# Kernel tuning notes

Hardware: AMD Instinct MI355X
Metric: run time of the kernel (lower is better)

Reference implementation:

```python
import jax, jax.numpy as jnp
import numpy as np
import math

V, S, E, H, L, B = 50257, 1024, 768, 12, 12, 4
D = E // H
EPS = 1e-5


def setup_inputs() -> dict:
    key = jax.random.key(0)
    ks = jax.random.split(key, 20)
    sd = 0.02
    inp = {
        "idx": jax.random.randint(ks[0], (B, S), 0, V),
        "targets": jax.random.randint(ks[1], (B, S), 0, V),
        "wte": jax.random.normal(ks[2], (V, E), jnp.float32) * sd,  # tied with lm_head
        "wpe": jax.random.normal(ks[3], (S, E), jnp.float32) * sd,
        "ln1_g": jnp.ones((L, E), jnp.float32),
        "ln1_b": jnp.zeros((L, E), jnp.float32),
        "attn_w": jax.random.normal(ks[4], (L, E, 3 * E), jnp.float32) * sd,
        "attn_b": jnp.zeros((L, 3 * E), jnp.float32),
        "proj_w": jax.random.normal(ks[5], (L, E, E), jnp.float32) * (sd / math.sqrt(2 * L)),
        "proj_b": jnp.zeros((L, E), jnp.float32),
        "ln2_g": jnp.ones((L, E), jnp.float32),
        "ln2_b": jnp.zeros((L, E), jnp.float32),
        "fc_w": jax.random.normal(ks[6], (L, E, 4 * E), jnp.float32) * sd,
        "fc_b": jnp.zeros((L, 4 * E), jnp.float32),
        "fcp_w": jax.random.normal(ks[7], (L, 4 * E, E), jnp.float32) * (sd / math.sqrt(2 * L)),
        "fcp_b": jnp.zeros((L, E), jnp.float32),
        "lnf_g": jnp.ones((E,), jnp.float32),
        "lnf_b": jnp.zeros((E,), jnp.float32),
    }
    return inp


def layer_norm(x, g, b):
    mu = jnp.mean(x, axis=-1, keepdims=True)
    var = jnp.mean(jnp.square(x - mu), axis=-1, keepdims=True)
    return (x - mu) * jax.lax.rsqrt(var + EPS) * g + b


def reference(idx, targets, wte, wpe, ln1_g, ln1_b, attn_w, attn_b, proj_w, proj_b,
              ln2_g, ln2_b, fc_w, fc_b, fcp_w, fcp_b, lnf_g, lnf_b):
    seq = idx.shape[1]
    x = wte[idx] + wpe[:seq]  # [B,S,E]
    mask = jnp.tril(jnp.ones((seq, seq), bool))
    scale = 1.0 / math.sqrt(D)

    def block(x, p):
        l1g, l1b, aw, ab, pw, pb, l2g, l2b, fw, fb, fpw, fpb = p
        h = layer_norm(x, l1g, l1b)
        qkv = h @ aw + ab  # [B,S,3E]
        q, k, v = jnp.split(qkv, 3, axis=-1)
        q = q.reshape(-1, seq, H, D).transpose(0, 2, 1, 3)  # [B,H,S,D]
        k = k.reshape(-1, seq, H, D).transpose(0, 2, 1, 3)
        v = v.reshape(-1, seq, H, D).transpose(0, 2, 1, 3)
        scores = jnp.einsum('bhqd,bhkd->bhqk', q, k) * scale
        scores = jnp.where(mask, scores, -jnp.inf)
        attn = jax.nn.softmax(scores, axis=-1)
        y = jnp.einsum('bhqk,bhkd->bhqd', attn, v)
        y = y.transpose(0, 2, 1, 3).reshape(-1, seq, E)
        x = x + y @ pw + pb
        h2 = layer_norm(x, l2g, l2b)
        h2 = jax.nn.gelu(h2 @ fw + fb, approximate=False)
        x = x + h2 @ fpw + fpb
        return x, None

    x, _ = jax.lax.scan(block, x, (ln1_g, ln1_b, attn_w, attn_b, proj_w, proj_b,
                                   ln2_g, ln2_b, fc_w, fc_b, fcp_w, fcp_b))
    x = layer_norm(x, lnf_g, lnf_b)
    logits = x @ wte.T  # tied lm_head, [B,S,V]
    logp = jax.nn.log_softmax(logits, axis=-1)
    loss = -jnp.mean(jnp.take_along_axis(logp, targets[..., None], axis=-1))
    return logits, loss
```

## Files before the change

kernel.cpp:

```cpp
#include <hip/hip_runtime.h>
#include <hip/hip_bf16.h>
#include <math.h>

#define V 50257
#define SQ 1024
#define E 768
#define NH 12
#define NL 12
#define NB 4
#define MR (NB*SQ)

typedef __bf16 bf16x8 __attribute__((ext_vector_type(8)));
typedef float f32x4 __attribute__((ext_vector_type(4)));
typedef unsigned short us8 __attribute__((ext_vector_type(8)));

__device__ __forceinline__ float b2f(unsigned short u) {
    union { float f; unsigned int i; } x; x.i = ((unsigned int)u) << 16; return x.f;
}
__device__ __forceinline__ unsigned short f2b(float f) {
    unsigned int u = __float_as_uint(f);
    u = (u + 0x7fff + ((u >> 16) & 1)) >> 16;
    return (unsigned short)u;
}
__device__ __forceinline__ void gload16(const unsigned short* g, unsigned short* l) {
    __builtin_amdgcn_global_load_lds((const __attribute__((address_space(1))) void*)g,
                                     (__attribute__((address_space(3))) void*)l, 16, 0, 0);
}

__global__ __launch_bounds__(256)
void embed_k(const int* __restrict__ idx, const float* __restrict__ wte,
             const float* __restrict__ wpe, float* __restrict__ x)
{
    int r = blockIdx.x, t = threadIdx.x;
    int tok = idx[r];
    int s = r & (SQ - 1);
    const float* wt = wte + (size_t)tok * E;
    const float* wp = wpe + (size_t)s * E;
    float* xr = x + (size_t)r * E;
    for (int e = t; e < E; e += 256) xr[e] = wt[e] + wp[e];
}

__global__ __launch_bounds__(256)
void ln_k(const float* __restrict__ x, const float* __restrict__ g,
          const float* __restrict__ bb, unsigned short* __restrict__ out)
{
    int r = blockIdx.x, t = threadIdx.x;
    int lane = t & 63, wid = t >> 6;
    const float* xr = x + (size_t)r * E;
    float v0 = xr[t], v1 = xr[t + 256], v2 = xr[t + 512];
    float s = v0 + v1 + v2;
    #pragma unroll
    for (int o = 1; o < 64; o <<= 1) s += __shfl_xor(s, o);
    __shared__ float red[8];
    if (lane == 0) red[wid] = s;
    __syncthreads();
    float mu = (red[0] + red[1] + red[2] + red[3]) * (1.f / E);
    float d0 = v0 - mu, d1 = v1 - mu, d2 = v2 - mu;
    float s2 = d0 * d0 + d1 * d1 + d2 * d2;
    #pragma unroll
    for (int o = 1; o < 64; o <<= 1) s2 += __shfl_xor(s2, o);
    if (lane == 0) red[wid + 4] = s2;
    __syncthreads();
    float rs = rsqrtf((red[4] + red[5] + red[6] + red[7]) * (1.f / E) + 1e-5f);
    unsigned short* orow = out + (size_t)r * E;
    orow[t]       = f2b(d0 * rs * g[t] + bb[t]);
    orow[t + 256] = f2b(d1 * rs * g[t + 256] + bb[t + 256]);
    orow[t + 512] = f2b(d2 * rs * g[t + 512] + bb[t + 512]);
}

__global__ __launch_bounds__(256)
void conv_k(const float* __restrict__ in, unsigned short* __restrict__ out, int n4)
{
    int i = blockIdx.x * 256 + threadIdx.x;
    int stride = gridDim.x * 256;
    for (; i < n4; i += stride) {
        float4 v = ((const float4*)in)[i];
        ushort4 o;
        o.x = f2b(v.x); o.y = f2b(v.y); o.z = f2b(v.z); o.w = f2b(v.w);
        ((ushort4*)out)[i] = o;
    }
}

__global__ __launch_bounds__(256)
void tconv_k(const float* __restrict__ in, unsigned short* __restrict__ out, int Kd, int Nd)
{
    __shared__ float tile[32][33];
    size_t loff = (size_t)blockIdx.z * Kd * Nd;
    in  += loff;
    out += loff;
    int n0 = blockIdx.x * 32, k0 = blockIdx.y * 32;
    int tc = threadIdx.x & 31, tr = threadIdx.x >> 5;
    #pragma unroll
    for (int i = 0; i < 4; ++i)
        tile[tr + i * 8][tc] = in[(size_t)(k0 + tr + i * 8) * Nd + n0 + tc];
    __syncthreads();
    #pragma unroll
    for (int i = 0; i < 4; ++i)
        out[(size_t)(n0 + tr + i * 8) * Kd + k0 + tc] = f2b(tile[tc][tr + i * 8]);
}

template<int EPI, bool DB>
__global__ __launch_bounds__(256, 3)
void gemm_k(const unsigned short* __restrict__ A, const unsigned short* __restrict__ B,
            const float* __restrict__ bias, const float* __restrict__ resid,
            void* __restrict__ Cv, unsigned short* __restrict__ vt,
            float2* __restrict__ part, int M, int N, int K, int Nreal)
{
    constexpr int NBUF = DB ? 2 : 1;
    __shared__ __align__(16) unsigned short As[NBUF][128 * 64];
    __shared__ __align__(16) unsigned short Bs[NBUF][128 * 64];
    const int t = threadIdx.x;
    const int lane = t & 63, wv = t >> 6;
    const int wr = wv >> 1, wc = wv & 1;

    int m0, n0, ntile;
    if constexpr (EPI == 3) {
        int lin = blockIdx.y * gridDim.x + blockIdx.x;
        int cpx = (gridDim.x * gridDim.y) >> 3;
        int nl  = (lin & 7) * cpx + (lin >> 3);
        int mt  = nl & (gridDim.x - 1);
        ntile   = nl / gridDim.x;
        m0 = mt * 128; n0 = ntile * 128;
    } else {
        m0 = blockIdx.x * 128; n0 = blockIdx.y * 128; ntile = blockIdx.y;
    }
    const int lq = lane & 15, lg = lane >> 4;

    f32x4 acc[4][4];
    const f32x4 fz = {0.f, 0.f, 0.f, 0.f};
    #pragma unroll
    for (int i = 0; i < 4; ++i)
        #pragma unroll
        for (int j = 0; j < 4; ++j) acc[i][j] = fz;

    const int srow = t >> 3, sc = t & 7;

    auto stage = [&](int buf, int k0) {
        #pragma unroll
        for (int i = 0; i < 4; ++i) {
            int row = srow + i * 32;
            int gc = ((sc ^ (row & 7)) << 3);
            gload16(A + (size_t)(m0 + row) * K + k0 + gc, &As[buf][row * 64 + sc * 8]);
            int nrow = n0 + row;
            if (EPI == 3 && nrow >= Nreal) nrow = Nreal - 1;
            gload16(B + (size_t)nrow * K + k0 + gc, &Bs[buf][row * 64 + sc * 8]);
        }
    };
    auto compute = [&](int buf) {
        #pragma unroll
        for (int ks = 0; ks < 64; ks += 32) {
            bf16x8 af[4], bfr[4];
            #pragma unroll
            for (int mi = 0; mi < 4; ++mi) {
                int row = wr * 64 + mi * 16 + lq;
                int c = (ks >> 3) + lg;
                af[mi] = *(const bf16x8*)&As[buf][row * 64 + ((c ^ (row & 7)) << 3)];
            }
            #pragma unroll
            for (int ni = 0; ni < 4; ++ni) {
                int row = wc * 64 + ni * 16 + lq;
                int c = (ks >> 3) + lg;
                bfr[ni] = *(const bf16x8*)&Bs[buf][row * 64 + ((c ^ (row & 7)) << 3)];
            }
            #pragma unroll
            for (int mi = 0; mi < 4; ++mi)
                #pragma unroll
                for (int ni = 0; ni < 4; ++ni)
                    acc[mi][ni] = __builtin_amdgcn_mfma_f32_16x16x32_bf16(
                        af[mi], bfr[ni], acc[mi][ni], 0, 0, 0);
        }
    };

    const int KT = K >> 6;
    if constexpr (DB) {
        stage(0, 0);
        __syncthreads();
        int cur = 0;
        for (int kt = 0; kt < KT; ++kt) {
            if (kt + 1 < KT) stage(cur ^ 1, (kt + 1) << 6);
            compute(cur);
            __syncthreads();
            cur ^= 1;
        }
    } else {
        for (int kt = 0; kt < KT; ++kt) {
            stage(0, kt << 6);
            __syncthreads();
            compute(0);
            __syncthreads();
        }
    }

    const int colb = n0 + wc * 64 + lq;
    const int rowb = m0 + wr * 64 + lg * 4;

    if constexpr (EPI == 3) {
        __shared__ float2 Ls[2][64][2];
        float* C = (float*)Cv;
        #pragma unroll
        for (int mi = 0; mi < 4; ++mi) {
            #pragma unroll
            for (int j = 0; j < 4; ++j) {
                int row = rowb + mi * 16 + j;
                float v[4];
                #pragma unroll
                for (int ni = 0; ni < 4; ++ni) {
                    int col = colb + ni * 16;
                    float vv = acc[mi][ni][j];
                    if (col < Nreal) C[(size_t)row * Nreal + col] = vv;
                    else vv = -1e30f;
                    v[ni] = vv;
                }
                float lm = fmaxf(fmaxf(v[0], v[1]), fmaxf(v[2], v[3]));
                #pragma unroll
                for (int o = 1; o < 16; o <<= 1) lm = fmaxf(lm, __shfl_xor(lm, o));
                float ls = __expf(v[0] - lm) + __expf(v[1] - lm)
                         + __expf(v[2] - lm) + __expf(v[3] - lm);
                #pragma unroll
                for (int o = 1; o < 16; o <<= 1) ls += __shfl_xor(ls, o);
                if (lq == 0) Ls[wr][mi * 16 + lg * 4 + j][wc] = make_float2(lm, ls);
            }
        }
        __syncthreads();
        if (t < 128) {
            float2 a = Ls[t >> 6][t & 63][0];
            float2 b = Ls[t >> 6][t & 63][1];
            float mm = fmaxf(a.x, b.x);
            float ss = a.y * __expf(a.x - mm) + b.y * __expf(b.x - mm);
            part[(size_t)ntile * MR + m0 + t] = make_float2(mm, ss);
        }
    } else if constexpr (EPI == 0) {
        unsigned short* C = (unsigned short*)Cv;
        #pragma unroll
        for (int mi = 0; mi < 4; ++mi) {
            int r0 = rowb + mi * 16;
            #pragma unroll
            for (int ni = 0; ni < 4; ++ni) {
                int col = colb + ni * 16;
                float b4 = bias[col];
                float vals[4];
                #pragma unroll
                for (int j = 0; j < 4; ++j) vals[j] = acc[mi][ni][j] + b4;
                #pragma unroll
                for (int j = 0; j < 4; ++j)
                    C[(size_t)(r0 + j) * N + col] = f2b(vals[j]);
                if (col >= 2 * E) {
                    int d = col - 2 * E; int hh = d >> 6; d &= 63;
                    int bb2 = r0 >> 10, kv = r0 & (SQ - 1);
                    unsigned int lo = (unsigned int)f2b(vals[0]) | ((unsigned int)f2b(vals[1]) << 16);
                    unsigned int hi = (unsigned int)f2b(vals[2]) | ((unsigned int)f2b(vals[3]) << 16);
                    uint2 u; u.x = lo; u.y = hi;
                    *(uint2*)&vt[(((size_t)bb2 * NH + hh) * 64 + d) * SQ + kv] = u;
                }
            }
        }
    } else {
        #pragma unroll
        for (int mi = 0; mi < 4; ++mi) {
            #pragma unroll
            for (int ni = 0; ni < 4; ++ni) {
                int col = colb + ni * 16;
                #pragma unroll
                for (int j = 0; j < 4; ++j) {
                    int row = rowb + mi * 16 + j;
                    float v = acc[mi][ni][j] + bias[col];
                    if constexpr (EPI == 1) {
                        ((float*)Cv)[(size_t)row * N + col] =
                            v + resid[(size_t)row * N + col];
                    } else {
                        float u = v + 0.044715f * v * v * v;
                        float e = __expf(-1.5957691216f * u);
                        v = v / (1.f + e);
                        ((unsigned short*)Cv)[(size_t)row * N + col] = f2b(v);
                    }
                }
            }
        }
    }
}

__global__ __launch_bounds__(256)
void attn_k(const unsigned short* __restrict__ qkv, const unsigned short* __restrict__ vtg,
            unsigned short* __restrict__ y)
{
    const int bid = blockIdx.x;
    const int qb  = (SQ / 64 - 1) - (bid / 48);
    const int bh  = bid % 48;
    const int h = bh % NH, b = bh / NH;
    const int t = threadIdx.x, lane = t & 63, wid = t >> 6;
    const int q0 = qb * 64;
    const int lq = lane & 15, lg = lane >> 4;

    __shared__ __align__(16) unsigned short Ks[64 * 72];
    __shared__ __align__(16) unsigned short Vs[64 * 72];
    __shared__ __align__(16) unsigned short Ps[4][16 * 72];

    const unsigned short* base  = qkv + (size_t)b * SQ * 2304;
    const unsigned short* vbase = vtg + (size_t)bh * 64 * SQ;

    const int qrow = q0 + wid * 16 + lq;
    bf16x8 qf0 = *(const bf16x8*)(base + (size_t)qrow * 2304 + h * 64 + lg * 8);
    bf16x8 qf1 = *(const bf16x8*)(base + (size_t)qrow * 2304 + h * 64 + 32 + lg * 8);

    const int sr = t >> 3, sc = t & 7;
    us8 ka, kb, va, vb;
    {
        const unsigned short* kp = base + (size_t)sr * 2304 + 768 + h * 64 + sc * 8;
        ka = *(const us8*)kp;
        kb = *(const us8*)(kp + (size_t)32 * 2304);
        const unsigned short* vp = vbase + (size_t)sr * SQ + sc * 8;
        va = *(const us8*)vp;
        vb = *(const us8*)(vp + (size_t)32 * SQ);
    }

    f32x4 of[4];
    const f32x4 fz = {0.f, 0.f, 0.f, 0.f};
    #pragma unroll
    for (int i = 0; i < 4; ++i) of[i] = fz;
    float mreg = -1e30f, lreg = 0.f;

    for (int tt = 0; tt <= qb; ++tt) {
        __syncthreads();
        *(us8*)&Ks[sr * 72 + sc * 8] = ka;
        *(us8*)&Ks[(sr + 32) * 72 + sc * 8] = kb;
        *(us8*)&Vs[sr * 72 + sc * 8] = va;
        *(us8*)&Vs[(sr + 32) * 72 + sc * 8] = vb;
        __syncthreads();
        if (tt < qb) {
            int kv0n = (tt + 1) * 64;
            const unsigned short* kp = base + (size_t)(kv0n + sr) * 2304 + 768 + h * 64 + sc * 8;
            ka = *(const us8*)kp;
            kb = *(const us8*)(kp + (size_t)32 * 2304);
            const unsigned short* vp = vbase + (size_t)sr * SQ + kv0n + sc * 8;
            va = *(const us8*)vp;
            vb = *(const us8*)(vp + (size_t)32 * SQ);
        }

        f32x4 sf[4];
        #pragma unroll
        for (int mi = 0; mi < 4; ++mi) sf[mi] = fz;
        #pragma unroll
        for (int mi = 0; mi < 4; ++mi) {
            const unsigned short* kr = &Ks[(mi * 16 + lq) * 72 + lg * 8];
            bf16x8 k0 = *(const bf16x8*)kr;
            bf16x8 k1 = *(const bf16x8*)(kr + 32);
            sf[mi] = __builtin_amdgcn_mfma_f32_16x16x32_bf16(k0, qf0, sf[mi], 0, 0, 0);
            sf[mi] = __builtin_amdgcn_mfma_f32_16x16x32_bf16(k1, qf1, sf[mi], 0, 0, 0);
        }

        float pv[16];
        const int kvb = tt * 64 + lg * 4;
        #pragma unroll
        for (int mi = 0; mi < 4; ++mi)
            #pragma unroll
            for (int j = 0; j < 4; ++j) {
                float s = sf[mi][j] * 0.125f;
                if (tt == qb && (kvb + mi * 16 + j) > qrow) s = -1e30f;
                pv[mi * 4 + j] = s;
            }
        float tm = pv[0];
        #pragma unroll
        for (int i = 1; i < 16; ++i) tm = fmaxf(tm, pv[i]);
        tm = fmaxf(tm, __shfl_xor(tm, 16));
        tm = fmaxf(tm, __shfl_xor(tm, 32));
        float mn  = fmaxf(mreg, tm);
        float fac = __expf(mreg - mn);
        float ts = 0.f;
        #pragma unroll
        for (int i = 0; i < 16; ++i) { float p = __expf(pv[i] - mn); pv[i] = p; ts += p; }
        ts += __shfl_xor(ts, 16);
        ts += __shfl_xor(ts, 32);
        lreg = lreg * fac + ts;
        mreg = mn;
        #pragma unroll
        for (int j = 0; j < 4; ++j) {
            float fj = __shfl(fac, 20 * lg + j);
            of[0][j] *= fj; of[1][j] *= fj; of[2][j] *= fj; of[3][j] *= fj;
        }
        unsigned short* pw = &Ps[wid][lq * 72];
        #pragma unroll
        for (int mi = 0; mi < 4; ++mi) {
            unsigned int lo = (unsigned int)f2b(pv[mi * 4 + 0]) | ((unsigned int)f2b(pv[mi * 4 + 1]) << 16);
            unsigned int hi = (unsigned int)f2b(pv[mi * 4 + 2]) | ((unsigned int)f2b(pv[mi * 4 + 3]) << 16);
            uint2 u; u.x = lo; u.y = hi;
            *(uint2*)&pw[mi * 16 + lg * 4] = u;
        }
        #pragma unroll
        for (int ks = 0; ks < 2; ++ks) {
            bf16x8 pf = *(const bf16x8*)&Ps[wid][lq * 72 + ks * 32 + lg * 8];
            #pragma unroll
            for (int ni = 0; ni < 4; ++ni) {
                bf16x8 vf = *(const bf16x8*)&Vs[(ni * 16 + lq) * 72 + ks * 32 + lg * 8];
                of[ni] = __builtin_amdgcn_mfma_f32_16x16x32_bf16(pf, vf, of[ni], 0, 0, 0);
            }
        }
    }

    float inv = 1.f / lreg;
    #pragma unroll
    for (int j = 0; j < 4; ++j) {
        float fj = __shfl(inv, 20 * lg + j);
        int row = q0 + wid * 16 + lg * 4 + j;
        unsigned short* yr = y + ((size_t)b * SQ + row) * E + h * 64 + lq;
        #pragma unroll
        for (int ni = 0; ni < 4; ++ni)
            yr[ni * 16] = f2b(of[ni][j] * fj);
    }
}

__global__ __launch_bounds__(256)
void lossred_k(const float2* __restrict__ part, const float* __restrict__ logits,
               const int* __restrict__ tgt, float* __restrict__ rl, int NT)
{
    int t = threadIdx.x, lane = t & 63, wid = t >> 6;
    int r = blockIdx.x * 4 + wid;
    float m = -1e30f, s = 0.f;
    for (int nt = lane; nt < NT; nt += 64) {
        float2 p = part[(size_t)nt * MR + r];
        float mm = fmaxf(m, p.x);
        s = s * __expf(m - mm) + p.y * __expf(p.x - mm);
        m = mm;
    }
    #pragma unroll
    for (int o = 1; o < 64; o <<= 1) {
        float m2 = __shfl_xor(m, o), s2 = __shfl_xor(s, o);
        float mm = fmaxf(m, m2);
        s = s * __expf(m - mm) + s2 * __expf(m2 - mm);
        m = mm;
    }
    if (lane == 0)
        rl[r] = __logf(s) + m - logits[(size_t)r * V + tgt[r]];
}

__global__ __launch_bounds__(256)
void finloss_k(const float* __restrict__ rl, float* __restrict__ out)
{
    __shared__ float red[256];
    int t = threadIdx.x;
    float s = 0.f;
    for (int i = t; i < MR; i += 256) s += rl[i];
    red[t] = s; __syncthreads();
    for (int o = 128; o > 0; o >>= 1) { if (t < o) red[t] += red[t + o]; __syncthreads(); }
    if (t == 0) out[0] = red[0] * (1.f / MR);
}

extern "C" void kernel_launch(void* const* d_in, const int* in_sizes, int n_in,
                              void* d_out, int out_size, void* d_ws, size_t ws_size,
                              hipStream_t stream)
{
    const int*   idx    = (const int*)  d_in[0];
    const int*   tgt    = (const int*)  d_in[1];
    const float* wte    = (const float*)d_in[2];
    const float* wpe    = (const float*)d_in[3];
    const float* ln1_g  = (const float*)d_in[4];
    const float* ln1_b  = (const float*)d_in[5];
    const float* attn_w = (const float*)d_in[6];
    const float* attn_b = (const float*)d_in[7];
    const float* proj_w = (const float*)d_in[8];
    const float* proj_b = (const float*)d_in[9];
    const float* ln2_g  = (const float*)d_in[10];
    const float* ln2_b  = (const float*)d_in[11];
    const float* fc_w   = (const float*)d_in[12];
    const float* fc_b   = (const float*)d_in[13];
    const float* fcp_w  = (const float*)d_in[14];
    const float* fcp_b  = (const float*)d_in[15];
    const float* lnf_g  = (const float*)d_in[16];
    const float* lnf_b  = (const float*)d_in[17];

    unsigned char* p = (unsigned char*)d_ws;
    auto alloc = [&](size_t bytes) {
        unsigned char* r = p; p += (bytes + 255) & ~(size_t)255; return r;
    };
    float*          x    = (float*)         alloc((size_t)MR * E * 4);
    unsigned short* h    = (unsigned short*)alloc((size_t)MR * E * 2);
    unsigned short* qkv  = (unsigned short*)alloc((size_t)MR * 3 * E * 2);
    unsigned short* yb   = (unsigned short*)alloc((size_t)MR * E * 2);
    unsigned short* act  = (unsigned short*)alloc((size_t)MR * 4 * E * 2);
    unsigned short* wteb = (unsigned short*)alloc((size_t)V * E * 2);
    unsigned short* vtg  = (unsigned short*)alloc((size_t)NB * NH * 64 * SQ * 2);
    float2*         part = (float2*)        alloc((size_t)393 * MR * 8);
    float*          rl   = (float*)         alloc((size_t)MR * 4);

    size_t used = (size_t)(p - (unsigned char*)d_ws);
    size_t perL = (size_t)12 * E * E * 2 + 4 * 256;
    int NLW = (ws_size >= used + (size_t)NL * perL) ? NL : 1;
    unsigned short* wqA  = (unsigned short*)alloc((size_t)NLW * 3 * E * E * 2);
    unsigned short* wpA  = (unsigned short*)alloc((size_t)NLW * E * E * 2);
    unsigned short* wfA  = (unsigned short*)alloc((size_t)NLW * 4 * E * E * 2);
    unsigned short* wfpA = (unsigned short*)alloc((size_t)NLW * 4 * E * E * 2);

    float* logits = (float*)d_out;
    float* lossp  = logits + (size_t)MR * V;

    embed_k<<<MR, 256, 0, stream>>>(idx, wte, wpe, x);
    conv_k<<<2048, 256, 0, stream>>>(wte, wteb, (int)((size_t)V * E / 4));

    if (NLW == NL) {
        tconv_k<<<dim3(3 * E / 32, E / 32, NL), 256, 0, stream>>>(attn_w, wqA, E, 3 * E);
        tconv_k<<<dim3(E / 32, E / 32, NL), 256, 0, stream>>>(proj_w, wpA, E, E);
        tconv_k<<<dim3(4 * E / 32, E / 32, NL), 256, 0, stream>>>(fc_w, wfA, E, 4 * E);
        tconv_k<<<dim3(E / 32, 4 * E / 32, NL), 256, 0, stream>>>(fcp_w, wfpA, 4 * E, E);
    }

    for (int l = 0; l < NL; ++l) {
        int lw = (NLW == NL) ? l : 0;
        unsigned short* wq  = wqA  + (size_t)lw * 3 * E * E;
        unsigned short* wp  = wpA  + (size_t)lw * E * E;
        unsigned short* wf  = wfA  + (size_t)lw * 4 * E * E;
        unsigned short* wfp = wfpA + (size_t)lw * 4 * E * E;
        if (NLW != NL) {
            tconv_k<<<dim3(3 * E / 32, E / 32), 256, 0, stream>>>(
                attn_w + (size_t)l * E * 3 * E, wq, E, 3 * E);
            tconv_k<<<dim3(E / 32, E / 32), 256, 0, stream>>>(
                proj_w + (size_t)l * E * E, wp, E, E);
            tconv_k<<<dim3(4 * E / 32, E / 32), 256, 0, stream>>>(
                fc_w + (size_t)l * E * 4 * E, wf, E, 4 * E);
            tconv_k<<<dim3(E / 32, 4 * E / 32), 256, 0, stream>>>(
                fcp_w + (size_t)l * 4 * E * E, wfp, 4 * E, E);
        }

        ln_k<<<MR, 256, 0, stream>>>(x, ln1_g + l * E, ln1_b + l * E, h);
        gemm_k<0, false><<<dim3(32, 18), 256, 0, stream>>>(
            h, wq, attn_b + (size_t)l * 3 * E, nullptr, qkv, vtg, nullptr,
            MR, 3 * E, E, 3 * E);
        attn_k<<<768, 256, 0, stream>>>(qkv, vtg, yb);
        gemm_k<1, false><<<dim3(32, 6), 256, 0, stream>>>(
            yb, wp, proj_b + (size_t)l * E, x, x, nullptr, nullptr, MR, E, E, E);
        ln_k<<<MR, 256, 0, stream>>>(x, ln2_g + l * E, ln2_b + l * E, h);
        gemm_k<2, false><<<dim3(32, 24), 256, 0, stream>>>(
            h, wf, fc_b + (size_t)l * 4 * E, nullptr, act, nullptr, nullptr,
            MR, 4 * E, E, 4 * E);
        gemm_k<1, false><<<dim3(32, 6), 256, 0, stream>>>(
            act, wfp, fcp_b + (size_t)l * E, x, x, nullptr, nullptr, MR, E, 4 * E, E);
    }

    ln_k<<<MR, 256, 0, stream>>>(x, lnf_g, lnf_b, h);
    gemm_k<3, true><<<dim3(32, 393), 256, 0, stream>>>(
        h, wteb, nullptr, nullptr, logits, nullptr, part, MR, 50304, E, V);

    lossred_k<<<MR / 4, 256, 0, stream>>>(part, logits, tgt, rl, 393);
    finloss_k<<<1, 256, 0, stream>>>(rl, lossp);
}
```

Measured before the change: 3.066 ms.

## Parameterize GEMM tile shape; use smaller tiles for projections and wider LM-head tiles

Templates the GEMM on per-wave MI/NI fragment counts and a min-waves launch bound, so each call site can pick its tile shape. The two N=768 projection GEMMs move to 64x128 tiles, doubling their block count to fill more CUs. The LM-head GEMM moves to 128x256 tiles without double buffering or the grouped tile swizzle, which halves the number of partial softmax entries and the A re-reads. The trade-off is higher register pressure (launch bound of 2) and the loss of L2-friendly tile ordering and load/compute overlap in the largest GEMM.

```diff
diff --git a/kernel.cpp b/kernel.cpp
--- a/kernel.cpp
+++ b/kernel.cpp
@@ -99,48 +99,44 @@
         out[(size_t)(n0 + tr + i * 8) * Kd + k0 + tc] = f2b(tile[tc][tr + i * 8]);
 }
 
-template<int EPI, bool DB>
-__global__ __launch_bounds__(256, 3)
+template<int EPI, bool DB, int MI, int NI, int MINW>
+__global__ __launch_bounds__(256, MINW)
 void gemm_k(const unsigned short* __restrict__ A, const unsigned short* __restrict__ B,
             const float* __restrict__ bias, const float* __restrict__ resid,
             void* __restrict__ Cv, unsigned short* __restrict__ vt,
             float2* __restrict__ part, int M, int N, int K, int Nreal)
 {
     constexpr int NBUF = DB ? 2 : 1;
-    __shared__ __align__(16) unsigned short As[NBUF][128 * 64];
-    __shared__ __align__(16) unsigned short Bs[NBUF][128 * 64];
+    constexpr int BM = 32 * MI, BN = 32 * NI;
+    __shared__ __align__(16) unsigned short As[NBUF][BM * 64];
+    __shared__ __align__(16) unsigned short Bs[NBUF][BN * 64];
     const int t = threadIdx.x;
     const int lane = t & 63, wv = t >> 6;
     const int wr = wv >> 1, wc = wv & 1;
-
-    int m0, n0, ntile;
-    if constexpr (EPI == 3) {
-        int lin = blockIdx.y * gridDim.x + blockIdx.x;
-        int cpx = (gridDim.x * gridDim.y) >> 3;
-        int nl  = (lin & 7) * cpx + (lin >> 3);
-        int mt  = nl & (gridDim.x - 1);
-        ntile   = nl / gridDim.x;
-        m0 = mt * 128; n0 = ntile * 128;
-    } else {
-        m0 = blockIdx.x * 128; n0 = blockIdx.y * 128; ntile = blockIdx.y;
-    }
+    const int m0 = blockIdx.x * BM, n0 = blockIdx.y * BN;
+    const int ntile = blockIdx.y;
     const int lq = lane & 15, lg = lane >> 4;
 
-    f32x4 acc[4][4];
+    f32x4 acc[MI][NI];
     const f32x4 fz = {0.f, 0.f, 0.f, 0.f};
     #pragma unroll
-    for (int i = 0; i < 4; ++i)
-        #pragma unroll
-        for (int j = 0; j < 4; ++j) acc[i][j] = fz;
+    for (int i = 0; i < MI; ++i)
+        #pragma unroll
+        for (int j = 0; j < NI; ++j) acc[i][j] = fz;
 
     const int srow = t >> 3, sc = t & 7;
 
     auto stage = [&](int buf, int k0) {
         #pragma unroll
-        for (int i = 0; i < 4; ++i) {
+        for (int i = 0; i < MI; ++i) {
             int row = srow + i * 32;
             int gc = ((sc ^ (row & 7)) << 3);
             gload16(A + (size_t)(m0 + row) * K + k0 + gc, &As[buf][row * 64 + sc * 8]);
+        }
+        #pragma unroll
+        for (int i = 0; i < NI; ++i) {
+            int row = srow + i * 32;
+            int gc = ((sc ^ (row & 7)) << 3);
             int nrow = n0 + row;
             if (EPI == 3 && nrow >= Nreal) nrow = Nreal - 1;
             gload16(B + (size_t)nrow * K + k0 + gc, &Bs[buf][row * 64 + sc * 8]);
@@ -149,23 +145,23 @@
     auto compute = [&](int buf) {
         #pragma unroll
         for (int ks = 0; ks < 64; ks += 32) {
-            bf16x8 af[4], bfr[4];
-            #pragma unroll
-            for (int mi = 0; mi < 4; ++mi) {
-                int row = wr * 64 + mi * 16 + lq;
+            bf16x8 af[MI], bfr[NI];
+            #pragma unroll
+            for (int mi = 0; mi < MI; ++mi) {
+                int row = wr * (16 * MI) + mi * 16 + lq;
                 int c = (ks >> 3) + lg;
                 af[mi] = *(const bf16x8*)&As[buf][row * 64 + ((c ^ (row & 7)) << 3)];
             }
             #pragma unroll
-            for (int ni = 0; ni < 4; ++ni) {
-                int row = wc * 64 + ni * 16 + lq;
+            for (int ni = 0; ni < NI; ++ni) {
+                int row = wc * (16 * NI) + ni * 16 + lq;
                 int c = (ks >> 3) + lg;
                 bfr[ni] = *(const bf16x8*)&Bs[buf][row * 64 + ((c ^ (row & 7)) << 3)];
             }
             #pragma unroll
-            for (int mi = 0; mi < 4; ++mi)
-                #pragma unroll
-                for (int ni = 0; ni < 4; ++ni)
+            for (int mi = 0; mi < MI; ++mi)
+                #pragma unroll
+                for (int ni = 0; ni < NI; ++ni)
                     acc[mi][ni] = __builtin_amdgcn_mfma_f32_16x16x32_bf16(
                         af[mi], bfr[ni], acc[mi][ni], 0, 0, 0);
         }
@@ -191,40 +187,43 @@
         }
     }
 
-    const int colb = n0 + wc * 64 + lq;
-    const int rowb = m0 + wr * 64 + lg * 4;
+    const int colb = n0 + wc * (16 * NI) + lq;
+    const int rowb = m0 + wr * (16 * MI) + lg * 4;
 
     if constexpr (EPI == 3) {
-        __shared__ float2 Ls[2][64][2];
+        __shared__ float2 Ls[2][BM / 2][2];
         float* C = (float*)Cv;
         #pragma unroll
-        for (int mi = 0; mi < 4; ++mi) {
+        for (int mi = 0; mi < MI; ++mi) {
             #pragma unroll
             for (int j = 0; j < 4; ++j) {
                 int row = rowb + mi * 16 + j;
-                float v[4];
-                #pragma unroll
-                for (int ni = 0; ni < 4; ++ni) {
+                float v[NI];
+                #pragma unroll
+                for (int ni = 0; ni < NI; ++ni) {
                     int col = colb + ni * 16;
                     float vv = acc[mi][ni][j];
                     if (col < Nreal) C[(size_t)row * Nreal + col] = vv;
                     else vv = -1e30f;
                     v[ni] = vv;
                 }
-                float lm = fmaxf(fmaxf(v[0], v[1]), fmaxf(v[2], v[3]));
+                float lm = v[0];
+                #pragma unroll
+                for (int ni = 1; ni < NI; ++ni) lm = fmaxf(lm, v[ni]);
                 #pragma unroll
                 for (int o = 1; o < 16; o <<= 1) lm = fmaxf(lm, __shfl_xor(lm, o));
-                float ls = __expf(v[0] - lm) + __expf(v[1] - lm)
-                         + __expf(v[2] - lm) + __expf(v[3] - lm);
+                float ls = 0.f;
+                #pragma unroll
+                for (int ni = 0; ni < NI; ++ni) ls += __expf(v[ni] - lm);
                 #pragma unroll
                 for (int o = 1; o < 16; o <<= 1) ls += __shfl_xor(ls, o);
                 if (lq == 0) Ls[wr][mi * 16 + lg * 4 + j][wc] = make_float2(lm, ls);
             }
         }
         __syncthreads();
-        if (t < 128) {
-            float2 a = Ls[t >> 6][t & 63][0];
-            float2 b = Ls[t >> 6][t & 63][1];
+        if (t < BM) {
+            float2 a = Ls[t / (BM / 2)][t % (BM / 2)][0];
+            float2 b = Ls[t / (BM / 2)][t % (BM / 2)][1];
             float mm = fmaxf(a.x, b.x);
             float ss = a.y * __expf(a.x - mm) + b.y * __expf(b.x - mm);
             part[(size_t)ntile * MR + m0 + t] = make_float2(mm, ss);
@@ -232,10 +231,10 @@
     } else if constexpr (EPI == 0) {
         unsigned short* C = (unsigned short*)Cv;
         #pragma unroll
-        for (int mi = 0; mi < 4; ++mi) {
+        for (int mi = 0; mi < MI; ++mi) {
             int r0 = rowb + mi * 16;
             #pragma unroll
-            for (int ni = 0; ni < 4; ++ni) {
+            for (int ni = 0; ni < NI; ++ni) {
                 int col = colb + ni * 16;
                 float b4 = bias[col];
                 float vals[4];
@@ -256,9 +255,9 @@
         }
     } else {
         #pragma unroll
-        for (int mi = 0; mi < 4; ++mi) {
-            #pragma unroll
-            for (int ni = 0; ni < 4; ++ni) {
+        for (int mi = 0; mi < MI; ++mi) {
+            #pragma unroll
+            for (int ni = 0; ni < NI; ++ni) {
                 int col = colb + ni * 16;
                 #pragma unroll
                 for (int j = 0; j < 4; ++j) {
@@ -478,7 +477,7 @@
     unsigned short* act  = (unsigned short*)alloc((size_t)MR * 4 * E * 2);
     unsigned short* wteb = (unsigned short*)alloc((size_t)V * E * 2);
     unsigned short* vtg  = (unsigned short*)alloc((size_t)NB * NH * 64 * SQ * 2);
-    float2*         part = (float2*)        alloc((size_t)393 * MR * 8);
+    float2*         part = (float2*)        alloc((size_t)197 * MR * 8);
     float*          rl   = (float*)         alloc((size_t)MR * 4);
 
     size_t used = (size_t)(p - (unsigned char*)d_ws);
@@ -520,24 +519,24 @@
         }
 
         ln_k<<<MR, 256, 0, stream>>>(x, ln1_g + l * E, ln1_b + l * E, h);
-        gemm_k<0, false><<<dim3(32, 18), 256, 0, stream>>>(
+        gemm_k<0, false, 4, 4, 3><<<dim3(32, 18), 256, 0, stream>>>(
             h, wq, attn_b + (size_t)l * 3 * E, nullptr, qkv, vtg, nullptr,
             MR, 3 * E, E, 3 * E);
         attn_k<<<768, 256, 0, stream>>>(qkv, vtg, yb);
-        gemm_k<1, false><<<dim3(32, 6), 256, 0, stream>>>(
+        gemm_k<1, false, 2, 4, 3><<<dim3(64, 6), 256, 0, stream>>>(
             yb, wp, proj_b + (size_t)l * E, x, x, nullptr, nullptr, MR, E, E, E);
         ln_k<<<MR, 256, 0, stream>>>(x, ln2_g + l * E, ln2_b + l * E, h);
-        gemm_k<2, false><<<dim3(32, 24), 256, 0, stream>>>(
+        gemm_k<2, false, 4, 4, 3><<<dim3(32, 24), 256, 0, stream>>>(
             h, wf, fc_b + (size_t)l * 4 * E, nullptr, act, nullptr, nullptr,
             MR, 4 * E, E, 4 * E);
-        gemm_k<1, false><<<dim3(32, 6), 256, 0, stream>>>(
+        gemm_k<1, false, 2, 4, 3><<<dim3(64, 6), 256, 0, stream>>>(
             act, wfp, fcp_b + (size_t)l * E, x, x, nullptr, nullptr, MR, E, 4 * E, E);
     }
 
     ln_k<<<MR, 256, 0, stream>>>(x, lnf_g, lnf_b, h);
-    gemm_k<3, true><<<dim3(32, 393), 256, 0, stream>>>(
+    gemm_k<3, false, 4, 8, 2><<<dim3(32, 197), 256, 0, stream>>>(
         h, wteb, nullptr, nullptr, logits, nullptr, part, MR, 50304, E, V);
 
-    lossred_k<<<MR / 4, 256, 0, stream>>>(part, logits, tgt, rl, 393);
+    lossred_k<<<MR / 4, 256, 0, stream>>>(part, logits, tgt, rl, 197);
     finloss_k<<<1, 256, 0, stream>>>(rl, lossp);
 }
```

After: 2.638 ms. 14.0% less time.
